# Kernel tuning notes

Hardware: AMD Instinct MI355X
Metric: run time of the kernel (lower is better)

## Reference

```python
import jax, jax.numpy as jnp
import numpy as np

B, T, E, D = 8, 4096, 64, 8  # batch, seq, embed_dim, head_dim (embed_dim//heads)


def setup_inputs() -> dict:
    key = jax.random.key(0)
    ks = jax.random.split(key, 7)
    scale = 1.0 / np.sqrt(E).astype(np.float32)
    return {
        "x": jax.random.normal(ks[0], (B, T, E), dtype=jnp.float32),
        "Wq": jax.random.normal(ks[1], (E, D), dtype=jnp.float32) * scale,
        "bq": jax.random.normal(ks[2], (D,), dtype=jnp.float32) * 0.01,
        "Wk": jax.random.normal(ks[3], (E, D), dtype=jnp.float32) * scale,
        "bk": jax.random.normal(ks[4], (D,), dtype=jnp.float32) * 0.01,
        "Wv": jax.random.normal(ks[5], (E, D), dtype=jnp.float32) * scale,
        "bv": jax.random.normal(ks[6], (D,), dtype=jnp.float32) * 0.01,
    }


def reference(x, Wq, bq, Wk, bk, Wv, bv):
    # q, k, v: [B, T, D]
    q = x @ Wq + bq
    k = x @ Wk + bk
    v = x @ Wv + bv
    b, t, d = k.shape
    # FAITHFUL to source: key(x).view(B, C, T) is a RESHAPE, not a transpose.
    w = q @ k.reshape(b, d, t)  # [B, T, T]
    # tril then masked_fill(w == 0, -inf): zero entries (incl. masked-out
    # upper triangle) become -inf before softmax.
    w = jnp.tril(w)
    w = jnp.where(w == 0, -jnp.inf, w)
    w = jax.nn.softmax(w / np.float32(np.sqrt(d)), axis=-1)
    return w @ v  # [B, T, D]
```

## Files before the change

### kernel.cpp

```cpp
#include <hip/hip_runtime.h>
#include <math.h>

#define BB 8
#define TT 4096
#define EE 64
#define DD 8
#define QSCALE 0.51012604f
#define CSHIFT -12.0f

typedef _Float16 half8  __attribute__((ext_vector_type(8)));
typedef _Float16 half4v __attribute__((ext_vector_type(4)));
typedef float    floatx4 __attribute__((ext_vector_type(4)));

#define VP_BATCH 65536

__global__ __launch_bounds__(256) void proj_kernel(
    const float* __restrict__ x,
    const float* __restrict__ Wq, const float* __restrict__ bq,
    const float* __restrict__ Wk, const float* __restrict__ bk,
    const float* __restrict__ Wv, const float* __restrict__ bv,
    _Float16* __restrict__ qh, _Float16* __restrict__ ks, _Float16* __restrict__ vP)
{
    __shared__ float    xs[32][EE + 1];
    __shared__ _Float16 qsm[256];
    __shared__ _Float16 ksm[256];
    __shared__ _Float16 vsm[256];

    const int tid   = threadIdx.x;
    const int blk   = blockIdx.x;
    const int b     = blk >> 7;
    const int tbase = (blk & 127) << 2;

#pragma unroll
    for (int m2 = 0; m2 < 2; ++m2) {
        int r = (tid >> 4) + (m2 << 4);
        int c = (tid & 15) << 2;
        int t = ((r >> 2) << 9) + tbase + (r & 3);
        float4 a = *(const float4*)(x + (size_t)(b * TT + t) * EE + c);
        xs[r][c+0] = a.x; xs[r][c+1] = a.y; xs[r][c+2] = a.z; xs[r][c+3] = a.w;
    }
    __syncthreads();

    const int r = tid >> 3;
    const int d = tid & 7;
    float accq = bq[d], acck = bk[d], accv = bv[d];
#pragma unroll
    for (int e = 0; e < EE; ++e) {
        float xv = xs[r][e];
        accq = fmaf(xv, Wq[e*DD + d], accq);
        acck = fmaf(xv, Wk[e*DD + d], acck);
        accv = fmaf(xv, Wv[e*DD + d], accv);
    }
    qsm[tid] = (_Float16)(accq * QSCALE);
    ksm[((r & 3) << 6) + (d << 3) + (r >> 2)] = (_Float16)acck;
    vsm[(d << 5) + r] = (_Float16)accv;
    __syncthreads();

    const int ilow = tbase >> 6;
    const int pv_  = (tbase >> 5) & 1;
    const int g2_  = (tbase >> 2) & 3;
    const int joff = (tbase & 16) ? 4 : 0;

    if (tid < 32) {
        half8 qv = *(half8*)(qsm + tid * 8);
        *(half8*)(qh + (size_t)b*(TT*DD) + (size_t)(tid >> 2)*(512*DD)
                     + (size_t)tbase*DD + ((tid & 3) << 3)) = qv;
        half8 kv = *(half8*)(ksm + tid * 8);
        *(half8*)(ks + (size_t)b*(TT*DD) + (size_t)tbase*64 + tid * 8) = kv;
    } else if (tid >= 64 && tid < 128) {
        int idx = tid - 64, d2 = idx >> 3, g2x = idx & 7;
        half4v vv = *(half4v*)(vsm + (d2 << 5) + (g2x << 2));
        const int i_ = (g2x << 3) + ilow;
        *(half4v*)(vP + (size_t)b*VP_BATCH + (size_t)i_*1024 + pv_*512
                      + (g2_ << 7) + (d2 << 3) + joff) = vv;
    } else if (tid >= 128 && tid < 136) {
        int g2x = tid & 7;
        const int i_ = (g2x << 3) + ilow;
        half4v ones = {(_Float16)1.0f, (_Float16)1.0f, (_Float16)1.0f, (_Float16)1.0f};
        *(half4v*)(vP + (size_t)b*VP_BATCH + (size_t)i_*1024 + pv_*512
                      + (g2_ << 7) + (8 << 3) + joff) = ones;
    }
}

__global__ __launch_bounds__(512, 4) void attn_kernel(
    const _Float16* __restrict__ qh, const _Float16* __restrict__ ks,
    const _Float16* __restrict__ vP, float* __restrict__ out)
{
    __shared__ floatx4 obuf[4][8][64];

    const int lane = threadIdx.x & 63;
    const int wave = threadIdx.x >> 6;
    const int g = lane >> 4;
    const int n = lane & 15;

    const int blk = blockIdx.x;
    const int bb  = blk & 7;
    const int p   = blk >> 3;
    const int r0A = p << 5;
    const int r0B = (127 - p) << 5;
    const int ntA = (p >> 1) + 1;
    const int ntB = ((255 - (p << 1)) >> 2) + 1;

    const _Float16* ksb = ks + (size_t)bb * (TT*DD);
    const _Float16* vPb = vP + (size_t)bb * VP_BATCH + (lane << 3);

    half8 qfA0, qfA1, qfB0, qfB1;
    {
        half8 z;
#pragma unroll
        for (int j = 0; j < 8; ++j) z[j] = (_Float16)0.0f;
        qfA0 = z; qfA1 = z; qfB0 = z; qfB1 = z;
        if (g == 0) {
            qfA0 = *(const half8*)(qh + ((size_t)bb*TT + r0A + n) * DD);
            qfA1 = *(const half8*)(qh + ((size_t)bb*TT + r0A + 16 + n) * DD);
            qfB0 = *(const half8*)(qh + ((size_t)bb*TT + r0B + n) * DD);
            qfB1 = *(const half8*)(qh + ((size_t)bb*TT + r0B + 16 + n) * DD);
        }
    }

    floatx4 oA0 = {0.f,0.f,0.f,0.f}, oA1 = {0.f,0.f,0.f,0.f};
    floatx4 oB0 = {0.f,0.f,0.f,0.f}, oB1 = {0.f,0.f,0.f,0.f};
    const floatx4 C12 = {CSHIFT, CSHIFT, CSHIFT, CSHIFT};

#define TILE_BODY(QF, R0, OACC)                                                 \
    {                                                                           \
        floatx4 S[4];                                                           \
        S[0] = __builtin_amdgcn_mfma_f32_16x16x32_f16(ck0, QF, C12, 0, 0, 0);   \
        S[1] = __builtin_amdgcn_mfma_f32_16x16x32_f16(ck1, QF, C12, 0, 0, 0);   \
        S[2] = __builtin_amdgcn_mfma_f32_16x16x32_f16(ck2, QF, C12, 0, 0, 0);   \
        S[3] = __builtin_amdgcn_mfma_f32_16x16x32_f16(ck3, QF, C12, 0, 0, 0);   \
        if (t2base + 63 > (R0)) {                                               \
            const int lim = (R0) + n - t2base - (g << 2);                       \
            _Pragma("unroll")                                                   \
            for (int s = 0; s < 4; ++s)                                         \
                _Pragma("unroll")                                               \
                for (int rr = 0; rr < 4; ++rr)                                  \
                    if ((s << 4) + rr > lim) S[s][rr] = -INFINITY;              \
        }                                                                       \
        int lo[4], hi[4];                                                       \
        _Pragma("unroll")                                                       \
        for (int s = 0; s < 4; ++s) {                                           \
            float p0 = __builtin_amdgcn_exp2f(S[s][0]);                         \
            float p1 = __builtin_amdgcn_exp2f(S[s][1]);                         \
            float p2 = __builtin_amdgcn_exp2f(S[s][2]);                         \
            float p3 = __builtin_amdgcn_exp2f(S[s][3]);                         \
            lo[s] = __builtin_bit_cast(int, __builtin_amdgcn_cvt_pkrtz(p0, p1));\
            hi[s] = __builtin_bit_cast(int, __builtin_amdgcn_cvt_pkrtz(p2, p3));\
        }                                                                       \
        {                                                                       \
            int4 bi; bi.x = lo[0]; bi.y = hi[0]; bi.z = lo[1]; bi.w = hi[1];    \
            half8 pb = __builtin_bit_cast(half8, bi);                           \
            OACC = __builtin_amdgcn_mfma_f32_16x16x32_f16(va0, pb, OACC, 0, 0, 0);\
        }                                                                       \
        {                                                                       \
            int4 bi; bi.x = lo[2]; bi.y = hi[2]; bi.z = lo[3]; bi.w = hi[3];    \
            half8 pb = __builtin_bit_cast(half8, bi);                           \
            OACC = __builtin_amdgcn_mfma_f32_16x16x32_f16(va1, pb, OACC, 0, 0, 0);\
        }                                                                       \
    }

#define ATTN_LOOP2(NT, R0LO, QF0, QF1, O0, O1)                                  \
    for (int i = wave; i < (NT); i += 8) {                                      \
        const int t2base = i << 6;                                              \
        const _Float16* kp = ksb + (size_t)(t2base + n) * DD;                   \
        half8 ck0 = *(const half8*)(kp);                                        \
        half8 ck1 = *(const half8*)(kp + 16 * DD);                              \
        half8 ck2 = *(const half8*)(kp + 32 * DD);                              \
        half8 ck3 = *(const half8*)(kp + 48 * DD);                              \
        half8 va0 = *(const half8*)(vPb + (size_t)i * 1024);                    \
        half8 va1 = *(const half8*)(vPb + (size_t)i * 1024 + 512);              \
        TILE_BODY(QF0, (R0LO), O0)                                              \
        TILE_BODY(QF1, (R0LO) + 16, O1)                                         \
    }

    ATTN_LOOP2(ntA, r0A, qfA0, qfA1, oA0, oA1)
    ATTN_LOOP2(ntB, r0B, qfB0, qfB1, oB0, oB1)
#undef ATTN_LOOP2
#undef TILE_BODY

    obuf[0][wave][lane] = oA0;
    obuf[1][wave][lane] = oA1;
    obuf[2][wave][lane] = oB0;
    obuf[3][wave][lane] = oB1;
    __syncthreads();

    if (wave < 4) {
        floatx4 osum = {0.f, 0.f, 0.f, 0.f};
#pragma unroll
        for (int w = 0; w < 8; ++w) osum += obuf[wave][w][lane];
        const float l    = __shfl(osum[0], 32 + n, 64);
        const float linv = 1.0f / l;
        const int   r0   = ((wave & 2) ? r0B : r0A) + ((wave & 1) << 4);
        if (g < 2) {
            float4 res;
            res.x = osum[0] * linv; res.y = osum[1] * linv;
            res.z = osum[2] * linv; res.w = osum[3] * linv;
            *(float4*)(out + (((size_t)bb * TT + r0 + n) * DD) + (g << 2)) = res;
        }
    }
}

extern "C" void kernel_launch(void* const* d_in, const int* in_sizes, int n_in,
                              void* d_out, int out_size, void* d_ws, size_t ws_size,
                              hipStream_t stream) {
    const float* x  = (const float*)d_in[0];
    const float* Wq = (const float*)d_in[1];
    const float* bq = (const float*)d_in[2];
    const float* Wk = (const float*)d_in[3];
    const float* bk = (const float*)d_in[4];
    const float* Wv = (const float*)d_in[5];
    const float* bv = (const float*)d_in[6];
    float* out = (float*)d_out;

    _Float16* qhp = (_Float16*)d_ws;
    _Float16* ksp = qhp + (size_t)BB * TT * DD;
    _Float16* vPp = ksp + (size_t)BB * TT * DD;

    proj_kernel<<<BB * TT / 32, 256, 0, stream>>>(x, Wq, bq, Wk, bk, Wv, bv, qhp, ksp, vPp);
    attn_kernel<<<512, 512, 0, stream>>>(qhp, ksp, vPp, out);
}
```

Baseline: 86.85 us.

## Process 64 query rows per half-block so each K/V tile feeds four query groups

Each attention block now handles two 64-row query strips (paired from both ends for causal load balance) instead of two 32-row strips, and the grid is halved to 256 blocks. Every K and V tile loaded per wave is reused across four 16-row query fragments instead of two, which halves global K/V traffic per unit of work. In exchange each wave holds more accumulators and Q fragments in registers, the LDS reduction buffer doubles, and only 256 blocks are launched, which may underfill the GPU's compute units.

```diff
diff --git a/kernel.cpp b/kernel.cpp
--- a/kernel.cpp
+++ b/kernel.cpp
@@ -86,7 +86,7 @@
     const _Float16* __restrict__ qh, const _Float16* __restrict__ ks,
     const _Float16* __restrict__ vP, float* __restrict__ out)
 {
-    __shared__ floatx4 obuf[4][8][64];
+    __shared__ floatx4 obuf[8][8][64];
 
     const int lane = threadIdx.x & 63;
     const int wave = threadIdx.x >> 6;
@@ -96,30 +96,36 @@
     const int blk = blockIdx.x;
     const int bb  = blk & 7;
     const int p   = blk >> 3;
-    const int r0A = p << 5;
-    const int r0B = (127 - p) << 5;
-    const int ntA = (p >> 1) + 1;
-    const int ntB = ((255 - (p << 1)) >> 2) + 1;
+    const int r0A = p << 6;
+    const int r0B = (63 - p) << 6;
+    const int ntA = p + 1;
+    const int ntB = 64 - p;
 
     const _Float16* ksb = ks + (size_t)bb * (TT*DD);
     const _Float16* vPb = vP + (size_t)bb * VP_BATCH + (lane << 3);
 
-    half8 qfA0, qfA1, qfB0, qfB1;
+    half8 qfA[4], qfB[4];
     {
         half8 z;
 #pragma unroll
         for (int j = 0; j < 8; ++j) z[j] = (_Float16)0.0f;
-        qfA0 = z; qfA1 = z; qfB0 = z; qfB1 = z;
+#pragma unroll
+        for (int q = 0; q < 4; ++q) { qfA[q] = z; qfB[q] = z; }
         if (g == 0) {
-            qfA0 = *(const half8*)(qh + ((size_t)bb*TT + r0A + n) * DD);
-            qfA1 = *(const half8*)(qh + ((size_t)bb*TT + r0A + 16 + n) * DD);
-            qfB0 = *(const half8*)(qh + ((size_t)bb*TT + r0B + n) * DD);
-            qfB1 = *(const half8*)(qh + ((size_t)bb*TT + r0B + 16 + n) * DD);
+#pragma unroll
+            for (int q = 0; q < 4; ++q) {
+                qfA[q] = *(const half8*)(qh + ((size_t)bb*TT + r0A + (q << 4) + n) * DD);
+                qfB[q] = *(const half8*)(qh + ((size_t)bb*TT + r0B + (q << 4) + n) * DD);
+            }
         }
     }
 
-    floatx4 oA0 = {0.f,0.f,0.f,0.f}, oA1 = {0.f,0.f,0.f,0.f};
-    floatx4 oB0 = {0.f,0.f,0.f,0.f}, oB1 = {0.f,0.f,0.f,0.f};
+    floatx4 oA[4], oB[4];
+#pragma unroll
+    for (int q = 0; q < 4; ++q) {
+        oA[q] = (floatx4){0.f,0.f,0.f,0.f};
+        oB[q] = (floatx4){0.f,0.f,0.f,0.f};
+    }
     const floatx4 C12 = {CSHIFT, CSHIFT, CSHIFT, CSHIFT};
 
 #define TILE_BODY(QF, R0, OACC)                                                 \
@@ -159,7 +165,7 @@
         }                                                                       \
     }
 
-#define ATTN_LOOP2(NT, R0LO, QF0, QF1, O0, O1)                                  \
+#define ATTN_LOOP4(NT, R0LO, QF, O)                                             \
     for (int i = wave; i < (NT); i += 8) {                                      \
         const int t2base = i << 6;                                              \
         const _Float16* kp = ksb + (size_t)(t2base + n) * DD;                   \
@@ -169,28 +175,32 @@
         half8 ck3 = *(const half8*)(kp + 48 * DD);                              \
         half8 va0 = *(const half8*)(vPb + (size_t)i * 1024);                    \
         half8 va1 = *(const half8*)(vPb + (size_t)i * 1024 + 512);              \
-        TILE_BODY(QF0, (R0LO), O0)                                              \
-        TILE_BODY(QF1, (R0LO) + 16, O1)                                         \
-    }
-
-    ATTN_LOOP2(ntA, r0A, qfA0, qfA1, oA0, oA1)
-    ATTN_LOOP2(ntB, r0B, qfB0, qfB1, oB0, oB1)
-#undef ATTN_LOOP2
+        TILE_BODY(QF[0], (R0LO), O[0])                                          \
+        TILE_BODY(QF[1], (R0LO) + 16, O[1])                                     \
+        TILE_BODY(QF[2], (R0LO) + 32, O[2])                                     \
+        TILE_BODY(QF[3], (R0LO) + 48, O[3])                                     \
+    }
+
+    ATTN_LOOP4(ntA, r0A, qfA, oA)
+    ATTN_LOOP4(ntB, r0B, qfB, oB)
+#undef ATTN_LOOP4
 #undef TILE_BODY
 
-    obuf[0][wave][lane] = oA0;
-    obuf[1][wave][lane] = oA1;
-    obuf[2][wave][lane] = oB0;
-    obuf[3][wave][lane] = oB1;
+#pragma unroll
+    for (int q = 0; q < 4; ++q) {
+        obuf[q][wave][lane]     = oA[q];
+        obuf[q + 4][wave][lane] = oB[q];
+    }
     __syncthreads();
 
-    if (wave < 4) {
+    {
         floatx4 osum = {0.f, 0.f, 0.f, 0.f};
 #pragma unroll
         for (int w = 0; w < 8; ++w) osum += obuf[wave][w][lane];
         const float l    = __shfl(osum[0], 32 + n, 64);
         const float linv = 1.0f / l;
-        const int   r0   = ((wave & 2) ? r0B : r0A) + ((wave & 1) << 4);
+        const int   r0   = (wave < 4) ? (r0A + (wave << 4))
+                                      : (r0B + ((wave - 4) << 4));
         if (g < 2) {
             float4 res;
             res.x = osum[0] * linv; res.y = osum[1] * linv;
@@ -217,5 +227,5 @@
     _Float16* vPp = ksp + (size_t)BB * TT * DD;
 
     proj_kernel<<<BB * TT / 32, 256, 0, stream>>>(x, Wq, bq, Wk, bk, Wv, bv, qhp, ksp, vPp);
-    attn_kernel<<<512, 512, 0, stream>>>(qhp, ksp, vPp, out);
+    attn_kernel<<<256, 512, 0, stream>>>(qhp, ksp, vPp, out);
 }
```

Result: no change. 87.18 us (+0.4%).
